# Kernel optimization log

Hardware: AMD Instinct MI355X
Metric: run time of the kernel (lower is better)

The kernel has to match this reference:

```python
import jax, jax.numpy as jnp
import numpy as np

B, T, DIM, LDIM, NAUX = 4096, 64, 16, 64, 32
H, AH = 256, 128
DT = 0.01
N_SHIFTS = 64
EPS = 1e-5


def _bn(x, g, b):
    # BatchNorm1d in training mode: batch stats, biased variance
    m = jnp.mean(x, 0)
    v = jnp.mean((x - m) ** 2, 0)
    return (x - m) / jnp.sqrt(v + EPS) * g + b


def _forward(xs, enc_bn_gamma, enc_bn_beta, enc_W1, enc_b1, enc_W2, enc_b2, enc_W3,
             enc_scale, aux_bn_gamma, aux_bn_beta, aux_W1, aux_b1, aux_W2, aux_b2,
             aux_W3, aux_scale, Cw):
    lrelu = jax.nn.leaky_relu  # negative_slope=0.01, matches F.leaky_relu default

    # ---- aux nets: 32 small MLPs on x0, vectorized over net index k ----
    x0 = xs[:, 0, :]                                   # [B, DIM]
    m = jnp.mean(x0, 0)
    v = jnp.mean((x0 - m) ** 2, 0)
    xn = (x0 - m) / jnp.sqrt(v + EPS)                  # shared batch stats
    xa = xn[None] * aux_bn_gamma[:, None, :] + aux_bn_beta[:, None, :]  # [K,B,DIM]
    h = lrelu(jnp.einsum('kbi,kji->kbj', xa, aux_W1) + aux_b1[:, None, :])
    h = lrelu(jnp.einsum('kbi,kji->kbj', h, aux_W2) + aux_b2[:, None, :])
    aux = (jnp.einsum('kbi,kji->kbj', h, aux_W3) * aux_scale[:, None, :])
    aux = aux.transpose(1, 0, 2)                       # [B, NAUX, 2] = (mu, omega)

    scale = jnp.exp(aux[..., 0] * DT)                  # [B, NAUX]
    cost = jnp.cos(aux[..., 1] * DT) * scale
    sint = jnp.sin(aux[..., 1] * DT) * scale

    # ---- encoder over trajectory ----
    xs_t = xs[:, :N_SHIFTS, :]                         # [B, T, DIM]
    xf = _bn(xs_t.reshape(-1, DIM), enc_bn_gamma, enc_bn_beta)
    hf = lrelu(xf @ enc_W1.T + enc_b1)
    hf = lrelu(hf @ enc_W2.T + enc_b2)
    yenc = ((hf @ enc_W3.T) * enc_scale).reshape(B, N_SHIFTS, LDIM)
    y = jnp.concatenate((xs_t, yenc), -1)              # [B, T, DIM+LDIM]

    # ---- Jordan-block Koopman recurrence: y @ blockdiag([[c,s],[-s,c]]) ----
    y0 = yenc[:, 0]                                    # [B, LDIM]

    def step(yc, _):
        yb = yc.reshape(B, NAUX, 2)
        o0 = cost * yb[..., 0] - sint * yb[..., 1]
        o1 = sint * yb[..., 0] + cost * yb[..., 1]
        yn = jnp.stack((o0, o1), -1).reshape(B, LDIM)
        return yn, (yn @ Cw.T, yn)

    _, (xseq, yseq) = jax.lax.scan(step, y0, None, length=N_SHIFTS - 1)
    x_pred = jnp.concatenate((xs_t[:, :1], xseq.transpose(1, 0, 2)), 1)   # [B,T,DIM]
    yl_pred = jnp.concatenate((y0[:, None], yseq.transpose(1, 0, 2)), 1)  # [B,T,LDIM]
    y_pred = jnp.concatenate((x_pred, yl_pred), -1)
    return y, y_pred


def setup_inputs() -> dict:
    key = jax.random.key(0)
    ks = jax.random.split(key, 10)
    r = lambda k, s, sc: jax.random.normal(k, s, jnp.float32) * sc
    return {
        'xs': jax.random.normal(ks[0], (B, T, DIM), jnp.float32),
        'enc_bn_gamma': jnp.ones((DIM,), jnp.float32),
        'enc_bn_beta': jnp.zeros((DIM,), jnp.float32),
        'enc_W1': r(ks[1], (H, DIM), 0.2),
        'enc_b1': jnp.zeros((H,), jnp.float32),
        'enc_W2': r(ks[2], (H, H), 0.06),
        'enc_b2': jnp.zeros((H,), jnp.float32),
        'enc_W3': r(ks[3], (LDIM, H), 0.06),
        'enc_scale': jnp.ones((LDIM,), jnp.float32),
        'aux_bn_gamma': jnp.ones((NAUX, DIM), jnp.float32),
        'aux_bn_beta': jnp.zeros((NAUX, DIM), jnp.float32),
        'aux_W1': r(ks[4], (NAUX, AH, DIM), 0.2),
        'aux_b1': jnp.zeros((NAUX, AH), jnp.float32),
        'aux_W2': r(ks[5], (NAUX, AH, AH), 0.09),
        'aux_b2': jnp.zeros((NAUX, AH), jnp.float32),
        'aux_W3': r(ks[6], (NAUX, 2, AH), 0.09),
        'aux_scale': jnp.ones((NAUX, 2), jnp.float32),
        'Cw': r(ks[7], (DIM, LDIM), 0.1),
    }


def reference(xs, enc_bn_gamma, enc_bn_beta, enc_W1, enc_b1, enc_W2, enc_b2, enc_W3,
              enc_scale, aux_bn_gamma, aux_bn_beta, aux_W1, aux_b1, aux_W2, aux_b2,
              aux_W3, aux_scale, Cw):
    return _forward(xs, enc_bn_gamma, enc_bn_beta, enc_W1, enc_b1, enc_W2, enc_b2,
                    enc_W3, enc_scale, aux_bn_gamma, aux_bn_beta, aux_W1, aux_b1,
                    aux_W2, aux_b2, aux_W3, aux_scale, Cw)
```

## Files before the change

### kernel.cpp

```cpp
#include <hip/hip_runtime.h>
#include <cstddef>

#define NBATCH 4096
#define NTIME  64
#define NDIM   16
#define NLDIM  64
#define NAUXK  32
#define NAH    128
#define NH     256
#define MROWS  (NBATCH*NTIME)
#define DT_C   0.01f
#define EPS_C  1e-5f
#define ENC_ITER 2
#define ENC_BLOCKS (MROWS/(64*ENC_ITER))
#define AUX_BLOCKS (NAUXK*64)

using short8 = __attribute__((ext_vector_type(8))) short;
using short4v = __attribute__((ext_vector_type(4))) short;
using f32x4 = __attribute__((ext_vector_type(4))) float;

__device__ __forceinline__ float lrelu(float x){ return fmaxf(x, 0.01f*x); }
__device__ __forceinline__ unsigned short f2bf(float f){
    unsigned u = __builtin_bit_cast(unsigned, f);
    u += 0x7fff + ((u>>16)&1u);
    return (unsigned short)(u>>16);
}
__device__ __forceinline__ unsigned cvt_pk(float a, float b){
    unsigned r;
    asm("v_cvt_pk_bf16_f32 %0, %1, %2" : "=v"(r) : "v"(a), "v"(b));
    return r;
}
__device__ __forceinline__ short4v pack4(f32x4 a){
    uint2 u;
    u.x = cvt_pk(lrelu(a[0]), lrelu(a[1]));
    u.y = cvt_pk(lrelu(a[2]), lrelu(a[3]));
    return __builtin_bit_cast(short4v, u);
}
__device__ __forceinline__ short4v pack4f(float x0,float x1,float x2,float x3){
    uint2 u;
    u.x = cvt_pk(x0, x1);
    u.y = cvt_pk(x2, x3);
    return __builtin_bit_cast(short4v, u);
}
#define HS2(m, idx) ((idx) ^ (((m)&15)<<2))

template<int STRIDE>
__device__ __forceinline__ short8 ld_h(const unsigned short* hb, int m, int c){
    short4v lo = *(const short4v*)&hb[HS2(m, m*STRIDE + c)];
    short4v hi = *(const short4v*)&hb[HS2(m, m*STRIDE + c + 4)];
    short8 r;
    r[0]=lo[0]; r[1]=lo[1]; r[2]=lo[2]; r[3]=lo[3];
    r[4]=hi[0]; r[5]=hi[1]; r[6]=hi[2]; r[7]=hi[3];
    return r;
}
template<int STRIDE>
__device__ __forceinline__ void st_h(unsigned short* hb, int m, int c, short4v p){
    *(short4v*)&hb[HS2(m, m*STRIDE + c)] = p;
}

__global__ __launch_bounds__(256) void k_mega1(const float* __restrict__ W1,
                                               const float* __restrict__ W2,
                                               const float* __restrict__ W3,
                                               const float* __restrict__ ag,
                                               const float* __restrict__ aW1,
                                               const float* __restrict__ aW2,
                                               const float* __restrict__ aW3,
                                               const float* __restrict__ ab1,
                                               const float* __restrict__ abt,
                                               const float* __restrict__ xs,
                                               unsigned short* __restrict__ dst,
                                               float* __restrict__ b1p,
                                               float* __restrict__ part){
    __shared__ float red[256*33];
    const int blk = blockIdx.x;
    const int tid = threadIdx.x;

    if(blk < 2896){
        int i = blk*256 + tid;
        float v;
        if(i < 4096){ v = W1[i]; }
        else if(i < 69632){
            int e = i - 4096;
            int kt = e>>13, r = e&8191;
            int rb = r>>9, sft = r&511;
            int l = sft>>3, j = sft&7;
            int g = l>>4, arw = l&15;
            v = W2[(rb*16+arw)*256 + kt*32 + g*8 + j];
        } else if(i < 86016){
            int e = i - 69632;
            int kt = e>>11, r = e&2047;
            int rb = r>>9, sft = r&511;
            int l = sft>>3, j = sft&7;
            int g = l>>4, arw = l&15;
            v = W3[(rb*16+arw)*256 + kt*32 + g*8 + j];
        } else if(i < 151552){
            int e = i - 86016; int k = e>>11, n = (e>>4)&127, c = e&15;
            v = aW1[(k*128+n)*16 + c] * ag[k*16+c];
        } else if(i < 675840){
            int e = i - 151552; int k = e>>14, kt = (e>>12)&3, n = (e>>5)&127, j = e&31;
            v = aW2[(k*128+n)*128 + kt*32 + j];
        } else if(i < 741376){
            int e = i - 675840; int k = e>>11, kt = (e>>9)&3, n = (e>>5)&15, j = e&31;
            v = (n < 2) ? aW3[(k*2+n)*128 + kt*32 + j] : 0.f;
        } else return;
        dst[i] = f2bf(v);
    } else if(blk < 2912){
        int i = (blk-2896)*256 + tid;
        int k = i>>7, n = i&127;
        const float* wr = aW1 + (size_t)(k*128+n)*16;
        const float* bt = abt + k*16;
        float a = ab1[i];
#pragma unroll
        for(int c=0;c<16;c++) a += wr[c]*bt[c];
        b1p[i] = a;
    } else {
        int sblk = blk - 2912;
        float s[16], q[16];
#pragma unroll
        for(int i=0;i<16;i++){ s[i]=0.f; q[i]=0.f; }
        int r0 = sblk*(MROWS/256) + tid;
        for(int j=0;j<4;j++){
            const float4* p = (const float4*)(xs + (size_t)(r0 + j*256)*NDIM);
#pragma unroll
            for(int v=0; v<4; v++){
                float4 f = p[v];
                s[v*4+0]+=f.x; q[v*4+0]+=f.x*f.x;
                s[v*4+1]+=f.y; q[v*4+1]+=f.y*f.y;
                s[v*4+2]+=f.z; q[v*4+2]+=f.z*f.z;
                s[v*4+3]+=f.w; q[v*4+3]+=f.w*f.w;
            }
        }
#pragma unroll
        for(int i=0;i<16;i++){ red[tid*33+i]=s[i]; red[tid*33+16+i]=q[i]; }
        __syncthreads();
        for(int off=128; off>0; off>>=1){
            if(tid < off){
#pragma unroll
                for(int i=0;i<32;i++) red[tid*33+i] += red[(tid+off)*33+i];
            }
            __syncthreads();
        }
        if(tid < 32) part[sblk*32 + tid] = red[tid];
    }
}

__global__ __launch_bounds__(256) void k_finalize(const float* __restrict__ xs,
                                                  const float* __restrict__ part,
                                                  const float* __restrict__ gamma,
                                                  const float* __restrict__ beta,
                                                  float* __restrict__ stats){
    __shared__ float red[256*33];
    __shared__ float x0tot[32];
    int tid = threadIdx.x;
    float s[16], q[16];
#pragma unroll
    for(int i=0;i<16;i++){ s[i]=0.f; q[i]=0.f; }
    for(int j=0;j<16;j++){
        int b = tid + j*256;
        const float4* p = (const float4*)(xs + (size_t)b*(NTIME*NDIM));
#pragma unroll
        for(int v=0; v<4; v++){
            float4 f = p[v];
            s[v*4+0]+=f.x; q[v*4+0]+=f.x*f.x;
            s[v*4+1]+=f.y; q[v*4+1]+=f.y*f.y;
            s[v*4+2]+=f.z; q[v*4+2]+=f.z*f.z;
            s[v*4+3]+=f.w; q[v*4+3]+=f.w*f.w;
        }
    }
#pragma unroll
    for(int i=0;i<16;i++){ red[tid*33+i]=s[i]; red[tid*33+16+i]=q[i]; }
    __syncthreads();
    for(int off=128; off>0; off>>=1){
        if(tid < off){
#pragma unroll
            for(int i=0;i<32;i++) red[tid*33+i] += red[(tid+off)*33+i];
        }
        __syncthreads();
    }
    if(tid < 32) x0tot[tid] = red[tid];
    __syncthreads();
#pragma unroll
    for(int i=0;i<32;i++) red[tid*33+i] = part[tid*32+i];
    __syncthreads();
    for(int off=128; off>0; off>>=1){
        if(tid < off){
#pragma unroll
            for(int i=0;i<32;i++) red[tid*33+i] += red[(tid+off)*33+i];
        }
        __syncthreads();
    }
    if(tid < 16){
        int i = tid;
        float m0 = x0tot[i] / (float)NBATCH;
        float v0 = x0tot[16+i] / (float)NBATCH - m0*m0;
        stats[32+i] = m0;
        stats[48+i] = 1.0f / sqrtf(v0 + EPS_C);
        float me = red[i] / (float)MROWS;
        float ve = red[16+i] / (float)MROWS - me*me;
        float a = gamma[i] / sqrtf(ve + EPS_C);
        stats[i]      = a;
        stats[16+i]   = beta[i] - me*a;
    }
}

__device__ __forceinline__ void enc_body(unsigned short* smem, int eb, int tid,
                                         const float* __restrict__ xs,
                                         const float* __restrict__ stats,
                                         const unsigned short* __restrict__ W1bf,
                                         const float* __restrict__ b1,
                                         const unsigned short* __restrict__ W2s,
                                         const float* __restrict__ b2,
                                         const unsigned short* __restrict__ W3s,
                                         const float* __restrict__ esc,
                                         float* __restrict__ outy){
    unsigned short* xa = smem;
    unsigned short* hb = smem + 1024;

    const int w    = tid >> 6;
    const int lane = tid & 63;
    const int g    = lane >> 4;
    const int arow = lane & 15;

    float4 sa = *(const float4*)&stats[(tid&3)*4];
    float4 sb = *(const float4*)&stats[16 + (tid&3)*4];

    const unsigned short* w2base = W2s + w*2048 + lane*8;
    const unsigned short* w3base = W3s + w*512 + lane*8;

    for(int it=0; it<ENC_ITER; it++){
        const int m0 = (eb*ENC_ITER + it)*64;

        short8 wcur[4];
#pragma unroll
        for(int nt=0; nt<4; nt++) wcur[nt] = *(const short8*)&w2base[nt*512];

        {
            int r = tid >> 2, c4 = (tid & 3)*4;
            float4 v = *(const float4*)(xs + (size_t)(m0 + r)*NDIM + c4);
            *(float4*)(outy + (size_t)(m0 + r)*80 + c4) = v;
            short4v p = pack4f(v.x*sa.x + sb.x, v.y*sa.y + sb.y,
                               v.z*sa.z + sb.z, v.w*sa.w + sb.w);
            *(short4v*)&xa[r*16 + c4] = p;
        }
        __syncthreads();

#pragma unroll
        for(int nt=0; nt<4; nt++){
            short8 aw = {0,0,0,0,0,0,0,0};
            if(lane < 32) aw = *(const short8*)&W1bf[(w*64 + nt*16 + arow)*16 + g*8];
            float4 b4 = *(const float4*)&b1[w*64 + nt*16 + g*4];
            f32x4 bi = {b4.x, b4.y, b4.z, b4.w};
#pragma unroll
            for(int mt=0; mt<4; mt++){
                short8 bx = {0,0,0,0,0,0,0,0};
                if(lane < 32) bx = *(const short8*)&xa[(mt*16 + arow)*16 + g*8];
                f32x4 a = __builtin_amdgcn_mfma_f32_16x16x32_bf16(aw, bx, bi, 0, 0, 0);
                st_h<256>(hb, mt*16 + arow, w*64 + nt*16 + g*4, pack4(a));
            }
        }
        __syncthreads();

        f32x4 acc[4][4];
#pragma unroll
        for(int nt=0; nt<4; nt++){
            float4 b4 = *(const float4*)&b2[w*64 + nt*16 + g*4];
            f32x4 bi = {b4.x, b4.y, b4.z, b4.w};
#pragma unroll
            for(int m=0;m<4;m++) acc[nt][m] = bi;
        }

#pragma unroll 1
        for(int kt=0; kt<8; kt++){
            short8 wnxt0={0,0,0,0,0,0,0,0}, wnxt1=wnxt0, wnxt2=wnxt0, wnxt3=wnxt0;
            if(kt < 7){
                const unsigned short* wp = w2base + (kt+1)*8192;
                wnxt0 = *(const short8*)&wp[0];
                wnxt1 = *(const short8*)&wp[512];
                wnxt2 = *(const short8*)&wp[1024];
                wnxt3 = *(const short8*)&wp[1536];
            }
#pragma unroll
            for(int mt=0; mt<4; mt++){
                short8 bh = ld_h<256>(hb, mt*16 + arow, kt*32 + g*8);
                acc[0][mt] = __builtin_amdgcn_mfma_f32_16x16x32_bf16(wcur[0], bh, acc[0][mt], 0, 0, 0);
                acc[1][mt] = __builtin_amdgcn_mfma_f32_16x16x32_bf16(wcur[1], bh, acc[1][mt], 0, 0, 0);
                acc[2][mt] = __builtin_amdgcn_mfma_f32_16x16x32_bf16(wcur[2], bh, acc[2][mt], 0, 0, 0);
                acc[3][mt] = __builtin_amdgcn_mfma_f32_16x16x32_bf16(wcur[3], bh, acc[3][mt], 0, 0, 0);
            }
            wcur[0]=wnxt0; wcur[1]=wnxt1; wcur[2]=wnxt2; wcur[3]=wnxt3;
        }
        __syncthreads();

#pragma unroll
        for(int nt=0; nt<4; nt++)
#pragma unroll
            for(int mt=0; mt<4; mt++)
                st_h<256>(hb, mt*16 + arow, w*64 + nt*16 + g*4, pack4(acc[nt][mt]));
        __syncthreads();

        f32x4 acc3[4];
#pragma unroll
        for(int m=0;m<4;m++) acc3[m] = (f32x4){0.f,0.f,0.f,0.f};
#pragma unroll 1
        for(int kt=0; kt<8; kt++){
            short8 aw3 = *(const short8*)&w3base[kt*2048];
#pragma unroll
            for(int mt=0; mt<4; mt++){
                short8 bh = ld_h<256>(hb, mt*16 + arow, kt*32 + g*8);
                acc3[mt] = __builtin_amdgcn_mfma_f32_16x16x32_bf16(aw3, bh, acc3[mt], 0, 0, 0);
            }
        }

        {
            float4 e4 = *(const float4*)&esc[w*16 + g*4];
#pragma unroll
            for(int mt=0; mt<4; mt++){
                float4 o;
                o.x = acc3[mt][0]*e4.x;
                o.y = acc3[mt][1]*e4.y;
                o.z = acc3[mt][2]*e4.z;
                o.w = acc3[mt][3]*e4.w;
                *(float4*)&outy[(size_t)(m0 + mt*16 + arow)*80 + 16 + w*16 + g*4] = o;
            }
        }
        if(it+1 < ENC_ITER) __syncthreads();
    }
}

__device__ __forceinline__ void aux_body(unsigned short* smem, int ab, int tid,
                                         const float* __restrict__ xs,
                                         const float* __restrict__ stats,
                                         const unsigned short* __restrict__ W1s,
                                         const float* __restrict__ b1p,
                                         const unsigned short* __restrict__ W2s,
                                         const float* __restrict__ ab2,
                                         const unsigned short* __restrict__ W3s,
                                         const float* __restrict__ asc,
                                         float* __restrict__ auxout){
    unsigned short* xa = smem;
    unsigned short* hb = smem + 1024;

    const int w    = tid >> 6;
    const int lane = tid & 63;
    const int g    = lane >> 4;
    const int arow = lane & 15;
    const int k    = ab >> 6;
    const int b0   = (ab & 63) * 64;

    short8 w1r[2], w2r[4][2], w3r[4];
#pragma unroll
    for(int nt=0; nt<2; nt++){
        short8 z = {0,0,0,0,0,0,0,0};
        if(lane < 32) z = *(const short8*)&W1s[(size_t)k*2048 + (w*32 + nt*16 + arow)*16 + g*8];
        w1r[nt] = z;
    }
#pragma unroll
    for(int kt=0; kt<4; kt++)
#pragma unroll
        for(int nt=0; nt<2; nt++)
            w2r[kt][nt] = *(const short8*)&W2s[(size_t)k*16384 + kt*4096 + (w*32 + nt*16 + arow)*32 + g*8];
#pragma unroll
    for(int kt=0; kt<4; kt++)
        w3r[kt] = *(const short8*)&W3s[(size_t)k*2048 + kt*512 + arow*32 + g*8];

    {
        int r = tid >> 2, c4 = (tid & 3)*4;
        float4 v = *(const float4*)(xs + (size_t)(b0 + r)*(NTIME*NDIM) + c4);
        short4v p = pack4f((v.x - stats[32+c4+0])*stats[48+c4+0],
                           (v.y - stats[32+c4+1])*stats[48+c4+1],
                           (v.z - stats[32+c4+2])*stats[48+c4+2],
                           (v.w - stats[32+c4+3])*stats[48+c4+3]);
        *(short4v*)&xa[r*16 + c4] = p;
    }
    __syncthreads();

#pragma unroll
    for(int nt=0; nt<2; nt++){
        float4 b4 = *(const float4*)&b1p[k*128 + w*32 + nt*16 + g*4];
        f32x4 bi = {b4.x, b4.y, b4.z, b4.w};
#pragma unroll
        for(int mt=0; mt<4; mt++){
            short8 bx = {0,0,0,0,0,0,0,0};
            if(lane < 32) bx = *(const short8*)&xa[(mt*16 + arow)*16 + g*8];
            f32x4 a = __builtin_amdgcn_mfma_f32_16x16x32_bf16(w1r[nt], bx, bi, 0, 0, 0);
            st_h<128>(hb, mt*16 + arow, w*32 + nt*16 + g*4, pack4(a));
        }
    }
    __syncthreads();

    f32x4 acc2[2][4];
#pragma unroll
    for(int nt=0; nt<2; nt++){
        float4 b4 = *(const float4*)&ab2[k*128 + w*32 + nt*16 + g*4];
        f32x4 bi = {b4.x, b4.y, b4.z, b4.w};
#pragma unroll
        for(int m=0;m<4;m++) acc2[nt][m] = bi;
    }

#pragma unroll
    for(int kt=0; kt<4; kt++){
        short8 bh[4];
#pragma unroll
        for(int mt=0; mt<4; mt++) bh[mt] = ld_h<128>(hb, mt*16 + arow, kt*32 + g*8);
#pragma unroll
        for(int nt=0; nt<2; nt++)
#pragma unroll
            for(int mt=0; mt<4; mt++)
                acc2[nt][mt] = __builtin_amdgcn_mfma_f32_16x16x32_bf16(w2r[kt][nt], bh[mt], acc2[nt][mt], 0, 0, 0);
    }
    __syncthreads();

#pragma unroll
    for(int nt=0; nt<2; nt++)
#pragma unroll
        for(int mt=0; mt<4; mt++)
            st_h<128>(hb, mt*16 + arow, w*32 + nt*16 + g*4, pack4(acc2[nt][mt]));
    __syncthreads();

    f32x4 acc3 = {0.f,0.f,0.f,0.f};
#pragma unroll
    for(int kt=0; kt<4; kt++){
        short8 bh = ld_h<128>(hb, w*16 + arow, kt*32 + g*8);
        acc3 = __builtin_amdgcn_mfma_f32_16x16x32_bf16(w3r[kt], bh, acc3, 0, 0, 0);
    }
    if(g == 0){
        float2 o;
        o.x = acc3[0] * asc[k*2+0] * DT_C;
        o.y = acc3[1] * asc[k*2+1] * DT_C;
        *(float2*)&auxout[(size_t)(b0 + w*16 + arow)*64 + 2*k] = o;
    }
}

__global__ __launch_bounds__(256) void k_mega2(const float* __restrict__ xs,
                                               const float* __restrict__ stats,
                                               const unsigned short* __restrict__ W1bf,
                                               const float* __restrict__ b1,
                                               const unsigned short* __restrict__ W2s,
                                               const float* __restrict__ b2,
                                               const unsigned short* __restrict__ W3s,
                                               const float* __restrict__ esc,
                                               const unsigned short* __restrict__ aW1s,
                                               const float* __restrict__ b1p,
                                               const unsigned short* __restrict__ aW2s,
                                               const float* __restrict__ ab2,
                                               const unsigned short* __restrict__ aW3s,
                                               const float* __restrict__ asc,
                                               float* __restrict__ outy,
                                               float* __restrict__ auxout){
    __shared__ unsigned short smem[17408];
    const int blk = blockIdx.x;
    const int tid = threadIdx.x;
    if(blk < ENC_BLOCKS){
        enc_body(smem, blk, tid, xs, stats, W1bf, b1, W2s, b2, W3s, esc, outy);
    } else {
        aux_body(smem, blk - ENC_BLOCKS, tid, xs, stats, aW1s, b1p, aW2s, ab2, aW3s, asc, auxout);
    }
}

__global__ __launch_bounds__(256) void k_pred(const float* __restrict__ xs,
                                              const float* __restrict__ auxbuf,
                                              const float* __restrict__ Cw,
                                              const float* __restrict__ outy,
                                              float* __restrict__ outyp){
    __shared__ float cw[16*64];
    const int tid = threadIdx.x;
    for(int j=tid; j<1024; j+=256) cw[j] = Cw[j];
    __syncthreads();

    int gid = blockIdx.x*256 + tid;
    int b = gid >> 6;
    int t = gid & 63;
    const float* yb = outy + (size_t)b*(NTIME*80) + 16;
    const float* ab = auxbuf + (size_t)b*64;
    float tt = (float)t;

    float y[64];
#pragma unroll
    for(int k=0;k<32;k++){
        float th0 = ab[2*k+0];
        float th1 = ab[2*k+1];
        float scl = __expf(th0*tt);
        float cc  = __cosf(th1*tt)*scl;
        float ss  = __sinf(th1*tt)*scl;
        float2 y01 = *(const float2*)&yb[2*k];
        y[2*k+0] = cc*y01.x - ss*y01.y;
        y[2*k+1] = ss*y01.x + cc*y01.y;
    }

    float* orow = outyp + (size_t)(b*NTIME + t)*80;
    if(t == 0){
        const float4* p = (const float4*)(xs + (size_t)b*(NTIME*NDIM));
#pragma unroll
        for(int i4=0;i4<4;i4++) *(float4*)&orow[i4*4] = p[i4];
    } else {
#pragma unroll
        for(int i4=0;i4<4;i4++){
            float o[4];
#pragma unroll
            for(int ii=0;ii<4;ii++){
                int i = i4*4+ii;
                float a = 0.f;
#pragma unroll
                for(int j4=0;j4<16;j4++){
                    float4 c4 = *(const float4*)&cw[i*64 + j4*4];
                    a += c4.x*y[j4*4+0] + c4.y*y[j4*4+1] + c4.z*y[j4*4+2] + c4.w*y[j4*4+3];
                }
                o[ii] = a;
            }
            *(float4*)&orow[i4*4] = make_float4(o[0],o[1],o[2],o[3]);
        }
    }
#pragma unroll
    for(int j4=0;j4<16;j4++){
        *(float4*)&orow[16+j4*4] = make_float4(y[j4*4+0],y[j4*4+1],y[j4*4+2],y[j4*4+3]);
    }
}

extern "C" void kernel_launch(void* const* d_in, const int* in_sizes, int n_in,
                              void* d_out, int out_size, void* d_ws, size_t ws_size,
                              hipStream_t stream) {
    const float* xs     = (const float*)d_in[0];
    const float* enc_g  = (const float*)d_in[1];
    const float* enc_bt = (const float*)d_in[2];
    const float* eW1    = (const float*)d_in[3];
    const float* eb1    = (const float*)d_in[4];
    const float* eW2    = (const float*)d_in[5];
    const float* eb2    = (const float*)d_in[6];
    const float* eW3    = (const float*)d_in[7];
    const float* esc    = (const float*)d_in[8];
    const float* ag     = (const float*)d_in[9];
    const float* abt    = (const float*)d_in[10];
    const float* aW1    = (const float*)d_in[11];
    const float* ab1    = (const float*)d_in[12];
    const float* aW2    = (const float*)d_in[13];
    const float* ab2    = (const float*)d_in[14];
    const float* aW3    = (const float*)d_in[15];
    const float* asc    = (const float*)d_in[16];
    const float* Cw     = (const float*)d_in[17];

    float* out   = (float*)d_out;
    float* ws    = (float*)d_ws;
    float* part   = ws;
    float* stats  = ws + 8192;
    float* auxout = ws + 8256;
    float* b1p    = ws + 270400;
    unsigned short* wbf = (unsigned short*)(ws + 274496);
    unsigned short* W1bf = wbf;
    unsigned short* W2s  = wbf + 4096;
    unsigned short* W3s  = wbf + 69632;
    unsigned short* aW1s = wbf + 86016;
    unsigned short* aW2s = wbf + 151552;
    unsigned short* aW3s = wbf + 675840;

    float* outy  = out;
    float* outyp = out + (size_t)NBATCH*NTIME*80;

    k_mega1<<<3168, 256, 0, stream>>>(eW1, eW2, eW3, ag, aW1, aW2, aW3,
                                      ab1, abt, xs, wbf, b1p, part);
    k_finalize<<<1, 256, 0, stream>>>(xs, part, enc_g, enc_bt, stats);
    k_mega2<<<ENC_BLOCKS + AUX_BLOCKS, 256, 0, stream>>>(
        xs, stats, W1bf, eb1, W2s, eb2, W3s, esc,
        aW1s, b1p, aW2s, ab2, aW3s, asc, outy, auxout);
    k_pred<<<MROWS/256, 256, 0, stream>>>(xs, auxout, Cw, outy, outyp);
}
```

Measured before the change: 157.9 us.

## Double mega2 block size to 512 threads and parallelize x0 stats reduction

The encoder and aux MLP kernel now runs 512-thread blocks, so each of 8 waves computes half as many output tiles per layer. Register accumulators per wave are halved, and the final aux layer runs on only 4 waves. The x0 batch-stat reduction moves out of the single-block finalize kernel into 16 extra blocks of the first kernel, so finalize only sums 16 partials. The goal is more latency hiding, lower register pressure, and a shorter serial finalize step, at the cost of more LDS syncs per block and fewer resident blocks.

```diff
diff --git a/kernel.cpp b/kernel.cpp
--- a/kernel.cpp
+++ b/kernel.cpp
@@ -36,12 +36,6 @@
     u.y = cvt_pk(lrelu(a[2]), lrelu(a[3]));
     return __builtin_bit_cast(short4v, u);
 }
-__device__ __forceinline__ short4v pack4f(float x0,float x1,float x2,float x3){
-    uint2 u;
-    u.x = cvt_pk(x0, x1);
-    u.y = cvt_pk(x2, x3);
-    return __builtin_bit_cast(short4v, u);
-}
 #define HS2(m, idx) ((idx) ^ (((m)&15)<<2))
 
 template<int STRIDE>
@@ -70,7 +64,8 @@
                                                const float* __restrict__ xs,
                                                unsigned short* __restrict__ dst,
                                                float* __restrict__ b1p,
-                                               float* __restrict__ part){
+                                               float* __restrict__ part,
+                                               float* __restrict__ part2){
     __shared__ float red[256*33];
     const int blk = blockIdx.x;
     const int tid = threadIdx.x;
@@ -113,7 +108,7 @@
 #pragma unroll
         for(int c=0;c<16;c++) a += wr[c]*bt[c];
         b1p[i] = a;
-    } else {
+    } else if(blk < 3168){
         int sblk = blk - 2912;
         float s[16], q[16];
 #pragma unroll
@@ -141,36 +136,42 @@
             __syncthreads();
         }
         if(tid < 32) part[sblk*32 + tid] = red[tid];
-    }
-}
-
-__global__ __launch_bounds__(256) void k_finalize(const float* __restrict__ xs,
-                                                  const float* __restrict__ part,
+    } else {
+        int sblk = blk - 3168;
+        int b = sblk*256 + tid;
+        const float4* p = (const float4*)(xs + (size_t)b*(NTIME*NDIM));
+#pragma unroll
+        for(int v=0; v<4; v++){
+            float4 f = p[v];
+            red[tid*33 + v*4+0] = f.x; red[tid*33+16 + v*4+0] = f.x*f.x;
+            red[tid*33 + v*4+1] = f.y; red[tid*33+16 + v*4+1] = f.y*f.y;
+            red[tid*33 + v*4+2] = f.z; red[tid*33+16 + v*4+2] = f.z*f.z;
+            red[tid*33 + v*4+3] = f.w; red[tid*33+16 + v*4+3] = f.w*f.w;
+        }
+        __syncthreads();
+        for(int off=128; off>0; off>>=1){
+            if(tid < off){
+#pragma unroll
+                for(int i=0;i<32;i++) red[tid*33+i] += red[(tid+off)*33+i];
+            }
+            __syncthreads();
+        }
+        if(tid < 32) part2[sblk*32 + tid] = red[tid];
+    }
+}
+
+__global__ __launch_bounds__(256) void k_finalize(const float* __restrict__ part,
+                                                  const float* __restrict__ part2,
                                                   const float* __restrict__ gamma,
                                                   const float* __restrict__ beta,
                                                   float* __restrict__ stats){
     __shared__ float red[256*33];
     __shared__ float x0tot[32];
     int tid = threadIdx.x;
-    float s[16], q[16];
-#pragma unroll
-    for(int i=0;i<16;i++){ s[i]=0.f; q[i]=0.f; }
-    for(int j=0;j<16;j++){
-        int b = tid + j*256;
-        const float4* p = (const float4*)(xs + (size_t)b*(NTIME*NDIM));
-#pragma unroll
-        for(int v=0; v<4; v++){
-            float4 f = p[v];
-            s[v*4+0]+=f.x; q[v*4+0]+=f.x*f.x;
-            s[v*4+1]+=f.y; q[v*4+1]+=f.y*f.y;
-            s[v*4+2]+=f.z; q[v*4+2]+=f.z*f.z;
-            s[v*4+3]+=f.w; q[v*4+3]+=f.w*f.w;
-        }
-    }
-#pragma unroll
-    for(int i=0;i<16;i++){ red[tid*33+i]=s[i]; red[tid*33+16+i]=q[i]; }
-    __syncthreads();
-    for(int off=128; off>0; off>>=1){
+#pragma unroll
+    for(int i=0;i<32;i++) red[tid*33+i] = (tid < 16) ? part2[tid*32+i] : 0.f;
+    __syncthreads();
+    for(int off=8; off>0; off>>=1){
         if(tid < off){
 #pragma unroll
             for(int i=0;i<32;i++) red[tid*33+i] += red[(tid+off)*33+i];
@@ -220,50 +221,52 @@
     const int lane = tid & 63;
     const int g    = lane >> 4;
     const int arow = lane & 15;
-
-    float4 sa = *(const float4*)&stats[(tid&3)*4];
-    float4 sb = *(const float4*)&stats[16 + (tid&3)*4];
-
-    const unsigned short* w2base = W2s + w*2048 + lane*8;
-    const unsigned short* w3base = W3s + w*512 + lane*8;
+    const int mh   = w & 1;
+    const int nt3  = w >> 1;
+
+    const int c2  = (tid & 7)*2;
+    const int r0p = tid >> 3;
+    const float sa0 = stats[c2],    sa1 = stats[c2+1];
+    const float sb0 = stats[16+c2], sb1 = stats[16+c2+1];
+
+    const unsigned short* w2base = W2s + (w*2)*512 + lane*8;
+    const unsigned short* w3base = W3s + nt3*512 + lane*8;
 
     for(int it=0; it<ENC_ITER; it++){
         const int m0 = (eb*ENC_ITER + it)*64;
 
-        short8 wcur[4];
-#pragma unroll
-        for(int nt=0; nt<4; nt++) wcur[nt] = *(const short8*)&w2base[nt*512];
+        short8 wcur[2];
+        wcur[0] = *(const short8*)&w2base[0];
+        wcur[1] = *(const short8*)&w2base[512];
 
         {
-            int r = tid >> 2, c4 = (tid & 3)*4;
-            float4 v = *(const float4*)(xs + (size_t)(m0 + r)*NDIM + c4);
-            *(float4*)(outy + (size_t)(m0 + r)*80 + c4) = v;
-            short4v p = pack4f(v.x*sa.x + sb.x, v.y*sa.y + sb.y,
-                               v.z*sa.z + sb.z, v.w*sa.w + sb.w);
-            *(short4v*)&xa[r*16 + c4] = p;
-        }
-        __syncthreads();
-
-#pragma unroll
-        for(int nt=0; nt<4; nt++){
+            float2 v = *(const float2*)(xs + (size_t)(m0 + r0p)*NDIM + c2);
+            *(float2*)(outy + (size_t)(m0 + r0p)*80 + c2) = v;
+            unsigned u = cvt_pk(v.x*sa0 + sb0, v.y*sa1 + sb1);
+            *(unsigned*)&xa[r0p*16 + c2] = u;
+        }
+        __syncthreads();
+
+#pragma unroll
+        for(int nt=0; nt<2; nt++){
             short8 aw = {0,0,0,0,0,0,0,0};
-            if(lane < 32) aw = *(const short8*)&W1bf[(w*64 + nt*16 + arow)*16 + g*8];
-            float4 b4 = *(const float4*)&b1[w*64 + nt*16 + g*4];
+            if(lane < 32) aw = *(const short8*)&W1bf[(w*32 + nt*16 + arow)*16 + g*8];
+            float4 b4 = *(const float4*)&b1[w*32 + nt*16 + g*4];
             f32x4 bi = {b4.x, b4.y, b4.z, b4.w};
 #pragma unroll
             for(int mt=0; mt<4; mt++){
                 short8 bx = {0,0,0,0,0,0,0,0};
                 if(lane < 32) bx = *(const short8*)&xa[(mt*16 + arow)*16 + g*8];
                 f32x4 a = __builtin_amdgcn_mfma_f32_16x16x32_bf16(aw, bx, bi, 0, 0, 0);
-                st_h<256>(hb, mt*16 + arow, w*64 + nt*16 + g*4, pack4(a));
-            }
-        }
-        __syncthreads();
-
-        f32x4 acc[4][4];
-#pragma unroll
-        for(int nt=0; nt<4; nt++){
-            float4 b4 = *(const float4*)&b2[w*64 + nt*16 + g*4];
+                st_h<256>(hb, mt*16 + arow, w*32 + nt*16 + g*4, pack4(a));
+            }
+        }
+        __syncthreads();
+
+        f32x4 acc[2][4];
+#pragma unroll
+        for(int nt=0; nt<2; nt++){
+            float4 b4 = *(const float4*)&b2[w*32 + nt*16 + g*4];
             f32x4 bi = {b4.x, b4.y, b4.z, b4.w};
 #pragma unroll
             for(int m=0;m<4;m++) acc[nt][m] = bi;
@@ -271,56 +274,55 @@
 
 #pragma unroll 1
         for(int kt=0; kt<8; kt++){
-            short8 wnxt0={0,0,0,0,0,0,0,0}, wnxt1=wnxt0, wnxt2=wnxt0, wnxt3=wnxt0;
+            short8 wn0={0,0,0,0,0,0,0,0}, wn1=wn0;
             if(kt < 7){
                 const unsigned short* wp = w2base + (kt+1)*8192;
-                wnxt0 = *(const short8*)&wp[0];
-                wnxt1 = *(const short8*)&wp[512];
-                wnxt2 = *(const short8*)&wp[1024];
-                wnxt3 = *(const short8*)&wp[1536];
+                wn0 = *(const short8*)&wp[0];
+                wn1 = *(const short8*)&wp[512];
             }
 #pragma unroll
             for(int mt=0; mt<4; mt++){
                 short8 bh = ld_h<256>(hb, mt*16 + arow, kt*32 + g*8);
                 acc[0][mt] = __builtin_amdgcn_mfma_f32_16x16x32_bf16(wcur[0], bh, acc[0][mt], 0, 0, 0);
                 acc[1][mt] = __builtin_amdgcn_mfma_f32_16x16x32_bf16(wcur[1], bh, acc[1][mt], 0, 0, 0);
-                acc[2][mt] = __builtin_amdgcn_mfma_f32_16x16x32_bf16(wcur[2], bh, acc[2][mt], 0, 0, 0);
-                acc[3][mt] = __builtin_amdgcn_mfma_f32_16x16x32_bf16(wcur[3], bh, acc[3][mt], 0, 0, 0);
-            }
-            wcur[0]=wnxt0; wcur[1]=wnxt1; wcur[2]=wnxt2; wcur[3]=wnxt3;
-        }
-        __syncthreads();
-
-#pragma unroll
-        for(int nt=0; nt<4; nt++)
+            }
+            wcur[0]=wn0; wcur[1]=wn1;
+        }
+        __syncthreads();
+
+#pragma unroll
+        for(int nt=0; nt<2; nt++)
 #pragma unroll
             for(int mt=0; mt<4; mt++)
-                st_h<256>(hb, mt*16 + arow, w*64 + nt*16 + g*4, pack4(acc[nt][mt]));
-        __syncthreads();
-
-        f32x4 acc3[4];
-#pragma unroll
-        for(int m=0;m<4;m++) acc3[m] = (f32x4){0.f,0.f,0.f,0.f};
+                st_h<256>(hb, mt*16 + arow, w*32 + nt*16 + g*4, pack4(acc[nt][mt]));
+        __syncthreads();
+
+        f32x4 acc3[2];
+        acc3[0] = (f32x4){0.f,0.f,0.f,0.f};
+        acc3[1] = (f32x4){0.f,0.f,0.f,0.f};
 #pragma unroll 1
         for(int kt=0; kt<8; kt++){
             short8 aw3 = *(const short8*)&w3base[kt*2048];
 #pragma unroll
-            for(int mt=0; mt<4; mt++){
+            for(int i=0;i<2;i++){
+                int mt = mh*2 + i;
                 short8 bh = ld_h<256>(hb, mt*16 + arow, kt*32 + g*8);
-                acc3[mt] = __builtin_amdgcn_mfma_f32_16x16x32_bf16(aw3, bh, acc3[mt], 0, 0, 0);
+                acc3[i] = __builtin_amdgcn_mfma_f32_16x16x32_bf16(aw3, bh, acc3[i], 0, 0, 0);
             }
         }
 
         {
-            float4 e4 = *(const float4*)&esc[w*16 + g*4];
-#pragma unroll
-            for(int mt=0; mt<4; mt++){
+            int nc = nt3*16 + g*4;
+            float4 e4 = *(const float4*)&esc[nc];
+#pragma unroll
+            for(int i=0;i<2;i++){
+                int mt = mh*2 + i;
                 float4 o;
-                o.x = acc3[mt][0]*e4.x;
-                o.y = acc3[mt][1]*e4.y;
-                o.z = acc3[mt][2]*e4.z;
-                o.w = acc3[mt][3]*e4.w;
-                *(float4*)&outy[(size_t)(m0 + mt*16 + arow)*80 + 16 + w*16 + g*4] = o;
+                o.x = acc3[i][0]*e4.x;
+                o.y = acc3[i][1]*e4.y;
+                o.z = acc3[i][2]*e4.z;
+                o.w = acc3[i][3]*e4.w;
+                *(float4*)&outy[(size_t)(m0 + mt*16 + arow)*80 + 16 + nc] = o;
             }
         }
         if(it+1 < ENC_ITER) __syncthreads();
@@ -347,91 +349,79 @@
     const int k    = ab >> 6;
     const int b0   = (ab & 63) * 64;
 
-    short8 w1r[2], w2r[4][2], w3r[4];
-#pragma unroll
-    for(int nt=0; nt<2; nt++){
-        short8 z = {0,0,0,0,0,0,0,0};
-        if(lane < 32) z = *(const short8*)&W1s[(size_t)k*2048 + (w*32 + nt*16 + arow)*16 + g*8];
-        w1r[nt] = z;
-    }
+    short8 w1r = {0,0,0,0,0,0,0,0};
+    if(lane < 32) w1r = *(const short8*)&W1s[(size_t)k*2048 + (w*16 + arow)*16 + g*8];
+    short8 w2r[4];
 #pragma unroll
     for(int kt=0; kt<4; kt++)
-#pragma unroll
-        for(int nt=0; nt<2; nt++)
-            w2r[kt][nt] = *(const short8*)&W2s[(size_t)k*16384 + kt*4096 + (w*32 + nt*16 + arow)*32 + g*8];
+        w2r[kt] = *(const short8*)&W2s[(size_t)k*16384 + kt*4096 + (w*16 + arow)*32 + g*8];
+    short8 w3r[4];
 #pragma unroll
     for(int kt=0; kt<4; kt++)
         w3r[kt] = *(const short8*)&W3s[(size_t)k*2048 + kt*512 + arow*32 + g*8];
 
     {
-        int r = tid >> 2, c4 = (tid & 3)*4;
-        float4 v = *(const float4*)(xs + (size_t)(b0 + r)*(NTIME*NDIM) + c4);
-        short4v p = pack4f((v.x - stats[32+c4+0])*stats[48+c4+0],
-                           (v.y - stats[32+c4+1])*stats[48+c4+1],
-                           (v.z - stats[32+c4+2])*stats[48+c4+2],
-                           (v.w - stats[32+c4+3])*stats[48+c4+3]);
-        *(short4v*)&xa[r*16 + c4] = p;
-    }
-    __syncthreads();
-
-#pragma unroll
-    for(int nt=0; nt<2; nt++){
-        float4 b4 = *(const float4*)&b1p[k*128 + w*32 + nt*16 + g*4];
+        const int c2  = (tid & 7)*2;
+        const int r0p = tid >> 3;
+        float2 v = *(const float2*)(xs + (size_t)(b0 + r0p)*(NTIME*NDIM) + c2);
+        unsigned u = cvt_pk((v.x - stats[32+c2])*stats[48+c2],
+                            (v.y - stats[32+c2+1])*stats[48+c2+1]);
+        *(unsigned*)&xa[r0p*16 + c2] = u;
+    }
+    __syncthreads();
+
+    {
+        float4 b4 = *(const float4*)&b1p[k*128 + w*16 + g*4];
         f32x4 bi = {b4.x, b4.y, b4.z, b4.w};
 #pragma unroll
         for(int mt=0; mt<4; mt++){
             short8 bx = {0,0,0,0,0,0,0,0};
             if(lane < 32) bx = *(const short8*)&xa[(mt*16 + arow)*16 + g*8];
-            f32x4 a = __builtin_amdgcn_mfma_f32_16x16x32_bf16(w1r[nt], bx, bi, 0, 0, 0);
-            st_h<128>(hb, mt*16 + arow, w*32 + nt*16 + g*4, pack4(a));
-        }
-    }
-    __syncthreads();
-
-    f32x4 acc2[2][4];
-#pragma unroll
-    for(int nt=0; nt<2; nt++){
-        float4 b4 = *(const float4*)&ab2[k*128 + w*32 + nt*16 + g*4];
+            f32x4 a = __builtin_amdgcn_mfma_f32_16x16x32_bf16(w1r, bx, bi, 0, 0, 0);
+            st_h<128>(hb, mt*16 + arow, w*16 + g*4, pack4(a));
+        }
+    }
+    __syncthreads();
+
+    f32x4 acc2[4];
+    {
+        float4 b4 = *(const float4*)&ab2[k*128 + w*16 + g*4];
         f32x4 bi = {b4.x, b4.y, b4.z, b4.w};
 #pragma unroll
-        for(int m=0;m<4;m++) acc2[nt][m] = bi;
-    }
-
+        for(int m=0;m<4;m++) acc2[m] = bi;
+    }
 #pragma unroll
     for(int kt=0; kt<4; kt++){
-        short8 bh[4];
-#pragma unroll
-        for(int mt=0; mt<4; mt++) bh[mt] = ld_h<128>(hb, mt*16 + arow, kt*32 + g*8);
-#pragma unroll
-        for(int nt=0; nt<2; nt++)
-#pragma unroll
-            for(int mt=0; mt<4; mt++)
-                acc2[nt][mt] = __builtin_amdgcn_mfma_f32_16x16x32_bf16(w2r[kt][nt], bh[mt], acc2[nt][mt], 0, 0, 0);
-    }
-    __syncthreads();
-
-#pragma unroll
-    for(int nt=0; nt<2; nt++)
-#pragma unroll
-        for(int mt=0; mt<4; mt++)
-            st_h<128>(hb, mt*16 + arow, w*32 + nt*16 + g*4, pack4(acc2[nt][mt]));
-    __syncthreads();
-
-    f32x4 acc3 = {0.f,0.f,0.f,0.f};
-#pragma unroll
-    for(int kt=0; kt<4; kt++){
-        short8 bh = ld_h<128>(hb, w*16 + arow, kt*32 + g*8);
-        acc3 = __builtin_amdgcn_mfma_f32_16x16x32_bf16(w3r[kt], bh, acc3, 0, 0, 0);
-    }
-    if(g == 0){
-        float2 o;
-        o.x = acc3[0] * asc[k*2+0] * DT_C;
-        o.y = acc3[1] * asc[k*2+1] * DT_C;
-        *(float2*)&auxout[(size_t)(b0 + w*16 + arow)*64 + 2*k] = o;
-    }
-}
-
-__global__ __launch_bounds__(256) void k_mega2(const float* __restrict__ xs,
+#pragma unroll
+        for(int mt=0; mt<4; mt++){
+            short8 bh = ld_h<128>(hb, mt*16 + arow, kt*32 + g*8);
+            acc2[mt] = __builtin_amdgcn_mfma_f32_16x16x32_bf16(w2r[kt], bh, acc2[mt], 0, 0, 0);
+        }
+    }
+    __syncthreads();
+
+#pragma unroll
+    for(int mt=0; mt<4; mt++)
+        st_h<128>(hb, mt*16 + arow, w*16 + g*4, pack4(acc2[mt]));
+    __syncthreads();
+
+    if(w < 4){
+        f32x4 acc3 = {0.f,0.f,0.f,0.f};
+#pragma unroll
+        for(int kt=0; kt<4; kt++){
+            short8 bh = ld_h<128>(hb, w*16 + arow, kt*32 + g*8);
+            acc3 = __builtin_amdgcn_mfma_f32_16x16x32_bf16(w3r[kt], bh, acc3, 0, 0, 0);
+        }
+        if(g == 0){
+            float2 o;
+            o.x = acc3[0] * asc[k*2+0] * DT_C;
+            o.y = acc3[1] * asc[k*2+1] * DT_C;
+            *(float2*)&auxout[(size_t)(b0 + w*16 + arow)*64 + 2*k] = o;
+        }
+    }
+}
+
+__global__ __launch_bounds__(512) void k_mega2(const float* __restrict__ xs,
                                                const float* __restrict__ stats,
                                                const unsigned short* __restrict__ W1bf,
                                                const float* __restrict__ b1,
@@ -542,9 +532,10 @@
     float* ws    = (float*)d_ws;
     float* part   = ws;
     float* stats  = ws + 8192;
-    float* auxout = ws + 8256;
-    float* b1p    = ws + 270400;
-    unsigned short* wbf = (unsigned short*)(ws + 274496);
+    float* part2  = ws + 8256;
+    float* auxout = ws + 8768;
+    float* b1p    = ws + 270912;
+    unsigned short* wbf = (unsigned short*)(ws + 275008);
     unsigned short* W1bf = wbf;
     unsigned short* W2s  = wbf + 4096;
     unsigned short* W3s  = wbf + 69632;
@@ -555,10 +546,10 @@
     float* outy  = out;
     float* outyp = out + (size_t)NBATCH*NTIME*80;
 
-    k_mega1<<<3168, 256, 0, stream>>>(eW1, eW2, eW3, ag, aW1, aW2, aW3,
-                                      ab1, abt, xs, wbf, b1p, part);
-    k_finalize<<<1, 256, 0, stream>>>(xs, part, enc_g, enc_bt, stats);
-    k_mega2<<<ENC_BLOCKS + AUX_BLOCKS, 256, 0, stream>>>(
+    k_mega1<<<3184, 256, 0, stream>>>(eW1, eW2, eW3, ag, aW1, aW2, aW3,
+                                      ab1, abt, xs, wbf, b1p, part, part2);
+    k_finalize<<<1, 256, 0, stream>>>(part, part2, enc_g, enc_bt, stats);
+    k_mega2<<<ENC_BLOCKS + AUX_BLOCKS, 512, 0, stream>>>(
         xs, stats, W1bf, eb1, W2s, eb2, W3s, esc,
         aW1s, b1p, aW2s, ab2, aW3s, asc, outy, auxout);
     k_pred<<<MROWS/256, 256, 0, stream>>>(xs, auxout, Cw, outy, outyp);
```

After: 145.2 us. 8.1% less time.
